# Kernel tuning notes

Measured on AMD Instinct MI355X. Metric: run time of the kernel, lower is better.

The kernel has to match this reference:

```python
import jax, jax.numpy as jnp
import numpy as np

KH, KW = 3, 3
KN = KH * KW  # kernel_n = 9


def _grid_offset(H, W):
    # Faithful to TF build(): stack(meshgrid(ij)).reshape(-1, 2) -- note this
    # interleaves i- and j- grids in an unusual layout; we replicate it exactly.
    init = jnp.stack(jnp.meshgrid(jnp.arange(KH), jnp.arange(KW), indexing='ij'))
    init = init.reshape(-1, 2).astype(jnp.float32)  # (KN, 2)
    ph, pw = (KH - 1) // 2, (KW - 1) // 2
    g = jnp.stack(
        jnp.meshgrid(jnp.arange(-ph, H - ph), jnp.arange(-pw, W - pw), indexing='ij'),
        axis=-1,
    ).astype(jnp.float32)  # (H, W, 2)
    return g[:, :, None, :] + init[None, None]  # (H, W, KN, 2)


def _bilinear_sample(x, coords):
    # x: (B, H, W, C); coords: (B, H, W, KN, 2) with (row, col) float coords.
    B = x.shape[0]
    y, xc = coords[..., 0], coords[..., 1]
    y0 = jnp.floor(y).astype(jnp.int32)
    y1 = jnp.ceil(y).astype(jnp.int32)   # ceil (not floor+1), faithful to TF code
    x0 = jnp.floor(xc).astype(jnp.int32)
    x1 = jnp.ceil(xc).astype(jnp.int32)
    bidx = jnp.arange(B)[:, None, None, None]

    def g(yy, xx):
        return x[bidx, yy, xx]  # (B, H, W, KN, C)

    v_lt = g(y0, x0)
    v_rb = g(y1, x1)
    v_lb = g(y0, x1)  # (lt_row, rb_col) per TF coords_lb
    v_rt = g(y1, x0)  # (rb_row, lt_col) per TF coords_rt
    fy = (y - y0.astype(y.dtype))[..., None]
    fx = (xc - x0.astype(xc.dtype))[..., None]
    v_t = v_lt + (v_rt - v_lt) * fy
    v_b = v_lb + (v_rb - v_lb) * fy
    return v_t + (v_b - v_t) * fx  # (B, H, W, KN, C)


def setup_inputs() -> dict:
    key = jax.random.key(0)
    k1, k2, k3 = jax.random.split(key, 3)
    B, H, W, C, F = 8, 64, 64, 128, 128
    x = jax.random.normal(k1, (B, H, W, C), dtype=jnp.float32)
    offset = jax.random.normal(k2, (B, H, W, 2 * KN), dtype=jnp.float32)
    Wk = jax.random.truncated_normal(k3, -2.0, 2.0, (KN, C, F), dtype=jnp.float32) * 0.02
    b = jnp.zeros((F,), dtype=jnp.float32)
    return {"x": x, "offset": offset, "W": Wk, "b": b}


def reference(x, offset, W, b):
    B, H, Wd, C = x.shape
    coords = _grid_offset(H, Wd)[None] + offset.reshape(B, H, Wd, KN, 2)
    coords = jnp.stack(
        [
            jnp.clip(coords[..., 0], 0.0, float(H - 1)),
            jnp.clip(coords[..., 1], 0.0, float(Wd - 1)),
        ],
        axis=-1,
    )
    deform = _bilinear_sample(x, coords)  # (B, H, W, KN, C)
    # conv3d with (1,1,KN,C,F) filter, VALID == contraction over (KN, C)
    out = jnp.einsum('bhwnc,ncf->bhwf', deform, W) + b
    return out
```

## Files before the change

kernel.cpp:

```cpp
#include <hip/hip_runtime.h>
#include <stdint.h>

#define KN 9
#define HH 64
#define WW 64
#define CC 128
#define FF 128
#define TM 64
#define NT 512
#define LDK 136

typedef __bf16 bf16x8 __attribute__((ext_vector_type(8)));
typedef float f32x4 __attribute__((ext_vector_type(4)));
typedef unsigned short us8 __attribute__((ext_vector_type(8)));
typedef unsigned short us4 __attribute__((ext_vector_type(4)));

__constant__ float c_init_i[KN] = {0.f,0.f,1.f,2.f,2.f,1.f,0.f,2.f,1.f};
__constant__ float c_init_j[KN] = {0.f,1.f,1.f,2.f,0.f,2.f,1.f,0.f,2.f};

static __device__ inline unsigned short f2bf(float f) {
    union { float f; unsigned u; } v; v.f = f;
    unsigned r = v.u + 0x7fffu + ((v.u >> 16) & 1u);
    return (unsigned short)(r >> 16);
}

__global__ void wt_kernel(const float* __restrict__ Wk, unsigned short* __restrict__ Wt) {
    __shared__ unsigned short t[32][33];
    const int tid = threadIdx.x;
    const int n  = blockIdx.x >> 4;
    const int tf = blockIdx.x & 3;
    const int tc = (blockIdx.x >> 2) & 3;
    const int g  = tid >> 5;
    const int l  = tid & 31;
#pragma unroll
    for (int r = 0; r < 4; ++r) {
        int cl = g * 4 + r;
        t[cl][l] = f2bf(Wk[(n << 14) + ((tc * 32 + cl) << 7) + (tf * 32 + l)]);
    }
    __syncthreads();
#pragma unroll
    for (int r = 0; r < 4; ++r) {
        int fl = g * 4 + r;
        Wt[(n << 14) + ((tf * 32 + fl) << 7) + (tc * 32 + l)] = t[l][fl];
    }
}

__launch_bounds__(NT, 4)
__global__ void deform_kernel(const float* __restrict__ xin,
                              const float* __restrict__ off,
                              const unsigned short* __restrict__ Wt,
                              const float* __restrict__ bias,
                              float* __restrict__ out) {
    __shared__ unsigned short As[TM][LDK];
    __shared__ unsigned short Bt[FF][LDK];
    __shared__ float cY[TM][KN];
    __shared__ float cX[TM][KN];

    const int tid = threadIdx.x;
    const int bb   = blockIdx.x & 7;
    const int hh   = blockIdx.x >> 3;
    const int pix0 = (bb << 12) + (hh << 6);

    for (int t = tid; t < TM * KN; t += NT) {
        int p = t & (TM - 1);
        int n = t >> 6;
        const float* op = off + (size_t)(pix0 + p) * (2 * KN) + 2 * n;
        float y = (float)(hh - 1) + c_init_i[n] + op[0];
        float x = (float)(p - 1) + c_init_j[n] + op[1];
        cY[p][n] = fminf(fmaxf(y, 0.f), 63.f);
        cX[p][n] = fminf(fmaxf(x, 0.f), 63.f);
    }
    __syncthreads();

    const int wave = tid >> 6;
    const int lane = tid & 63;
    const int quad = lane >> 4;
    const int col  = lane & 15;
    const int mtile = (wave & 1) * 32;
    const int ntile = (wave >> 1) * 32;

    f32x4 acc[2][2];
#pragma unroll
    for (int a = 0; a < 2; ++a)
#pragma unroll
        for (int b = 0; b < 2; ++b) acc[a][b] = (f32x4){0.f, 0.f, 0.f, 0.f};

    const float* bbase = xin + ((size_t)bb << 19);

    auto issue_gather = [&](int n, int k, float4* pf) {
        int i  = tid + k * NT;
        int p  = i >> 5;
        int cg = (i & 31) * 4;
        float y = cY[p][n], x = cX[p][n];
        int y0 = (int)floorf(y), x0 = (int)floorf(x);
        int y1 = (int)ceilf(y),  x1 = (int)ceilf(x);
        pf[0] = *(const float4*)(bbase + ((((y0 << 6) + x0) << 7) + cg));
        pf[1] = *(const float4*)(bbase + ((((y1 << 6) + x0) << 7) + cg));
        pf[2] = *(const float4*)(bbase + ((((y0 << 6) + x1) << 7) + cg));
        pf[3] = *(const float4*)(bbase + ((((y1 << 6) + x1) << 7) + cg));
    };
    auto consume = [&](int n, int k, const float4* pf) {
        int i  = tid + k * NT;
        int p  = i >> 5;
        int cg = (i & 31) * 4;
        float y = cY[p][n], x = cX[p][n];
        float fy = y - floorf(y), fx = x - floorf(x);
        float r0, r1, r2, r3;
        { float vt = pf[0].x + (pf[1].x - pf[0].x) * fy; float vb = pf[2].x + (pf[3].x - pf[2].x) * fy; r0 = vt + (vb - vt) * fx; }
        { float vt = pf[0].y + (pf[1].y - pf[0].y) * fy; float vb = pf[2].y + (pf[3].y - pf[2].y) * fy; r1 = vt + (vb - vt) * fx; }
        { float vt = pf[0].z + (pf[1].z - pf[0].z) * fy; float vb = pf[2].z + (pf[3].z - pf[2].z) * fy; r2 = vt + (vb - vt) * fx; }
        { float vt = pf[0].w + (pf[1].w - pf[0].w) * fy; float vb = pf[2].w + (pf[3].w - pf[2].w) * fy; r3 = vt + (vb - vt) * fx; }
        us4 pk;
        pk.x = f2bf(r0); pk.y = f2bf(r1); pk.z = f2bf(r2); pk.w = f2bf(r3);
        *(us4*)&As[p][cg] = pk;
    };

    float4 pf0[4], pf1[4];
    us8 bpf[4];
    issue_gather(0, 0, pf0);
    issue_gather(0, 1, pf1);
#pragma unroll
    for (int k = 0; k < 4; ++k) {
        int i2 = tid + k * NT;
        bpf[k] = *(const us8*)(Wt + (i2 >> 4) * CC + (i2 & 15) * 8);
    }

    for (int n = 0; n < KN; ++n) {
        float4 pf2[4], pf3[4];
        issue_gather(n, 2, pf2);
        issue_gather(n, 3, pf3);
#pragma unroll
        for (int k = 0; k < 4; ++k) {
            int i2 = tid + k * NT;
            *(us8*)&Bt[i2 >> 4][(i2 & 15) * 8] = bpf[k];
        }
        consume(n, 0, pf0);
        consume(n, 1, pf1);
        consume(n, 2, pf2);
        consume(n, 3, pf3);
        __syncthreads();

        if (n + 1 < KN) {
            issue_gather(n + 1, 0, pf0);
            issue_gather(n + 1, 1, pf1);
            const unsigned short* Wn = Wt + (n + 1) * (CC * FF);
#pragma unroll
            for (int k = 0; k < 4; ++k) {
                int i2 = tid + k * NT;
                bpf[k] = *(const us8*)(Wn + (i2 >> 4) * CC + (i2 & 15) * 8);
            }
        }

#pragma unroll
        for (int ks = 0; ks < 4; ++ks) {
            bf16x8 a0 = __builtin_bit_cast(bf16x8, *(const us8*)(&As[mtile + col][ks * 32 + quad * 8]));
            bf16x8 a1 = __builtin_bit_cast(bf16x8, *(const us8*)(&As[mtile + 16 + col][ks * 32 + quad * 8]));
            bf16x8 b0 = __builtin_bit_cast(bf16x8, *(const us8*)(&Bt[ntile + col][ks * 32 + quad * 8]));
            bf16x8 b1 = __builtin_bit_cast(bf16x8, *(const us8*)(&Bt[ntile + 16 + col][ks * 32 + quad * 8]));
            acc[0][0] = __builtin_amdgcn_mfma_f32_16x16x32_bf16(a0, b0, acc[0][0], 0, 0, 0);
            acc[0][1] = __builtin_amdgcn_mfma_f32_16x16x32_bf16(a0, b1, acc[0][1], 0, 0, 0);
            acc[1][0] = __builtin_amdgcn_mfma_f32_16x16x32_bf16(a1, b0, acc[1][0], 0, 0, 0);
            acc[1][1] = __builtin_amdgcn_mfma_f32_16x16x32_bf16(a1, b1, acc[1][1], 0, 0, 0);
        }
        __syncthreads();
    }

#pragma unroll
    for (int b = 0; b < 2; ++b) {
        int f = ntile + b * 16 + col;
        float bv = bias[f];
#pragma unroll
        for (int a = 0; a < 2; ++a) {
#pragma unroll
            for (int r = 0; r < 4; ++r) {
                int pr = pix0 + mtile + a * 16 + quad * 4 + r;
                out[(size_t)pr * FF + f] = acc[a][b][r] + bv;
            }
        }
    }
}

extern "C" void kernel_launch(void* const* d_in, const int* in_sizes, int n_in,
                              void* d_out, int out_size, void* d_ws, size_t ws_size,
                              hipStream_t stream) {
    const float* x    = (const float*)d_in[0];
    const float* off  = (const float*)d_in[1];
    const float* Wk   = (const float*)d_in[2];
    const float* bias = (const float*)d_in[3];
    float* out = (float*)d_out;
    unsigned short* Wt = (unsigned short*)d_ws;

    wt_kernel<<<KN * 16, 256, 0, stream>>>(Wk, Wt);
    deform_kernel<<<(8 * HH * WW) / TM, NT, 0, stream>>>(x, off, Wt, bias, out);
}
```

Baseline: 105.3 us.

## Load weights directly into registers and precompute gather offsets per tap

Repacks the bf16 weight workspace so each wave reads its MFMA B fragments straight from global memory into registers, which removes the shared-memory Bt tile and the store/read round trip through it. Corner offsets and fractional weights are now computed once in the prologue and kept in shared memory, so the gather loop no longer repeats floor/ceil per tap. Each thread now handles 8 channels of 2 pixels instead of 4 channels of 4 pixels, and uses native bf16 conversion. Less shared memory may allow more blocks per CU. In exchange, register pressure rises (16 float4 prefetch values plus 8 weight vectors), and the weight loads are now exposed in the main loop without prefetching across taps.

```diff
diff --git a/kernel.cpp b/kernel.cpp
--- a/kernel.cpp
+++ b/kernel.cpp
@@ -13,7 +13,6 @@
 typedef __bf16 bf16x8 __attribute__((ext_vector_type(8)));
 typedef float f32x4 __attribute__((ext_vector_type(4)));
 typedef unsigned short us8 __attribute__((ext_vector_type(8)));
-typedef unsigned short us4 __attribute__((ext_vector_type(4)));
 
 __constant__ float c_init_i[KN] = {0.f,0.f,1.f,2.f,2.f,1.f,0.f,2.f,1.f};
 __constant__ float c_init_j[KN] = {0.f,1.f,1.f,2.f,0.f,2.f,1.f,0.f,2.f};
@@ -41,7 +40,7 @@
 #pragma unroll
     for (int r = 0; r < 4; ++r) {
         int fl = g * 4 + r;
-        Wt[(n << 14) + ((tf * 32 + fl) << 7) + (tc * 32 + l)] = t[l][fl];
+        Wt[(n << 14) + (tc << 12) + ((tf * 32 + fl) << 5) + l] = t[l][fl];
     }
 }
 
@@ -52,9 +51,8 @@
                               const float* __restrict__ bias,
                               float* __restrict__ out) {
     __shared__ unsigned short As[TM][LDK];
-    __shared__ unsigned short Bt[FF][LDK];
-    __shared__ float cY[TM][KN];
-    __shared__ float cX[TM][KN];
+    __shared__ int   cB[TM][KN][4];
+    __shared__ float cF[TM][KN][2];
 
     const int tid = threadIdx.x;
     const int bb   = blockIdx.x & 7;
@@ -67,10 +65,18 @@
         const float* op = off + (size_t)(pix0 + p) * (2 * KN) + 2 * n;
         float y = (float)(hh - 1) + c_init_i[n] + op[0];
         float x = (float)(p - 1) + c_init_j[n] + op[1];
-        cY[p][n] = fminf(fmaxf(y, 0.f), 63.f);
-        cX[p][n] = fminf(fmaxf(x, 0.f), 63.f);
+        y = fminf(fmaxf(y, 0.f), 63.f);
+        x = fminf(fmaxf(x, 0.f), 63.f);
+        float y0f = floorf(y), x0f = floorf(x);
+        int y0 = (int)y0f, x0 = (int)x0f;
+        int y1 = (int)ceilf(y), x1 = (int)ceilf(x);
+        cB[p][n][0] = ((y0 << 6) + x0) << 7;
+        cB[p][n][1] = ((y1 << 6) + x0) << 7;
+        cB[p][n][2] = ((y0 << 6) + x1) << 7;
+        cB[p][n][3] = ((y1 << 6) + x1) << 7;
+        cF[p][n][0] = y - y0f;
+        cF[p][n][1] = x - x0f;
     }
-    __syncthreads();
 
     const int wave = tid >> 6;
     const int lane = tid & 63;
@@ -86,77 +92,66 @@
         for (int b = 0; b < 2; ++b) acc[a][b] = (f32x4){0.f, 0.f, 0.f, 0.f};
 
     const float* bbase = xin + ((size_t)bb << 19);
+    const unsigned short* wb0 = Wt + ((ntile + col) << 5) + (quad << 3);
 
-    auto issue_gather = [&](int n, int k, float4* pf) {
-        int i  = tid + k * NT;
-        int p  = i >> 5;
-        int cg = (i & 31) * 4;
-        float y = cY[p][n], x = cX[p][n];
-        int y0 = (int)floorf(y), x0 = (int)floorf(x);
-        int y1 = (int)ceilf(y),  x1 = (int)ceilf(x);
-        pf[0] = *(const float4*)(bbase + ((((y0 << 6) + x0) << 7) + cg));
-        pf[1] = *(const float4*)(bbase + ((((y1 << 6) + x0) << 7) + cg));
-        pf[2] = *(const float4*)(bbase + ((((y0 << 6) + x1) << 7) + cg));
-        pf[3] = *(const float4*)(bbase + ((((y1 << 6) + x1) << 7) + cg));
+    const int ip0 = tid >> 4;
+    const int ip1 = ip0 + 32;
+    const int icg = (tid & 15) * 8;
+
+    auto issue = [&](int n, int p, float4* pf) {
+        int4 cb = *(const int4*)&cB[p][n][0];
+        const float* c0 = bbase + cb.x + icg;
+        const float* c1 = bbase + cb.y + icg;
+        const float* c2 = bbase + cb.z + icg;
+        const float* c3 = bbase + cb.w + icg;
+        pf[0] = *(const float4*)c0; pf[1] = *(const float4*)(c0 + 4);
+        pf[2] = *(const float4*)c1; pf[3] = *(const float4*)(c1 + 4);
+        pf[4] = *(const float4*)c2; pf[5] = *(const float4*)(c2 + 4);
+        pf[6] = *(const float4*)c3; pf[7] = *(const float4*)(c3 + 4);
     };
-    auto consume = [&](int n, int k, const float4* pf) {
-        int i  = tid + k * NT;
-        int p  = i >> 5;
-        int cg = (i & 31) * 4;
-        float y = cY[p][n], x = cX[p][n];
-        float fy = y - floorf(y), fx = x - floorf(x);
-        float r0, r1, r2, r3;
-        { float vt = pf[0].x + (pf[1].x - pf[0].x) * fy; float vb = pf[2].x + (pf[3].x - pf[2].x) * fy; r0 = vt + (vb - vt) * fx; }
-        { float vt = pf[0].y + (pf[1].y - pf[0].y) * fy; float vb = pf[2].y + (pf[3].y - pf[2].y) * fy; r1 = vt + (vb - vt) * fx; }
-        { float vt = pf[0].z + (pf[1].z - pf[0].z) * fy; float vb = pf[2].z + (pf[3].z - pf[2].z) * fy; r2 = vt + (vb - vt) * fx; }
-        { float vt = pf[0].w + (pf[1].w - pf[0].w) * fy; float vb = pf[2].w + (pf[3].w - pf[2].w) * fy; r3 = vt + (vb - vt) * fx; }
-        us4 pk;
-        pk.x = f2bf(r0); pk.y = f2bf(r1); pk.z = f2bf(r2); pk.w = f2bf(r3);
-        *(us4*)&As[p][cg] = pk;
+    auto consume = [&](int n, int p, const float4* pf) {
+        float fy = cF[p][n][0], fx = cF[p][n][1];
+        us8 pk;
+#pragma unroll
+        for (int j = 0; j < 8; ++j) {
+            float v0 = pf[0 + (j >> 2)][j & 3];
+            float v1 = pf[2 + (j >> 2)][j & 3];
+            float v2 = pf[4 + (j >> 2)][j & 3];
+            float v3 = pf[6 + (j >> 2)][j & 3];
+            float vt = v0 + (v1 - v0) * fy;
+            float vb = v2 + (v3 - v2) * fy;
+            float r  = vt + (vb - vt) * fx;
+            pk[j] = __builtin_bit_cast(unsigned short, (__bf16)r);
+        }
+        *(us8*)&As[p][icg] = pk;
     };
 
-    float4 pf0[4], pf1[4];
-    us8 bpf[4];
-    issue_gather(0, 0, pf0);
-    issue_gather(0, 1, pf1);
-#pragma unroll
-    for (int k = 0; k < 4; ++k) {
-        int i2 = tid + k * NT;
-        bpf[k] = *(const us8*)(Wt + (i2 >> 4) * CC + (i2 & 15) * 8);
-    }
+    __syncthreads();
+
+    float4 pf0[8], pf1[8];
+    us8 bfr[8];
+    issue(0, ip0, pf0);
 
     for (int n = 0; n < KN; ++n) {
-        float4 pf2[4], pf3[4];
-        issue_gather(n, 2, pf2);
-        issue_gather(n, 3, pf3);
+        const unsigned short* wn = wb0 + (n << 14);
 #pragma unroll
-        for (int k = 0; k < 4; ++k) {
-            int i2 = tid + k * NT;
-            *(us8*)&Bt[i2 >> 4][(i2 & 15) * 8] = bpf[k];
+        for (int ks = 0; ks < 4; ++ks) {
+            bfr[ks * 2]     = *(const us8*)(wn + (ks << 12));
+            bfr[ks * 2 + 1] = *(const us8*)(wn + (ks << 12) + (16 << 5));
         }
-        consume(n, 0, pf0);
-        consume(n, 1, pf1);
-        consume(n, 2, pf2);
-        consume(n, 3, pf3);
+        issue(n, ip1, pf1);
+        consume(n, ip0, pf0);
+        consume(n, ip1, pf1);
         __syncthreads();
 
-        if (n + 1 < KN) {
-            issue_gather(n + 1, 0, pf0);
-            issue_gather(n + 1, 1, pf1);
-            const unsigned short* Wn = Wt + (n + 1) * (CC * FF);
-#pragma unroll
-            for (int k = 0; k < 4; ++k) {
-                int i2 = tid + k * NT;
-                bpf[k] = *(const us8*)(Wn + (i2 >> 4) * CC + (i2 & 15) * 8);
-            }
-        }
+        if (n + 1 < KN) issue(n + 1, ip0, pf0);
 
 #pragma unroll
         for (int ks = 0; ks < 4; ++ks) {
             bf16x8 a0 = __builtin_bit_cast(bf16x8, *(const us8*)(&As[mtile + col][ks * 32 + quad * 8]));
             bf16x8 a1 = __builtin_bit_cast(bf16x8, *(const us8*)(&As[mtile + 16 + col][ks * 32 + quad * 8]));
-            bf16x8 b0 = __builtin_bit_cast(bf16x8, *(const us8*)(&Bt[ntile + col][ks * 32 + quad * 8]));
-            bf16x8 b1 = __builtin_bit_cast(bf16x8, *(const us8*)(&Bt[ntile + 16 + col][ks * 32 + quad * 8]));
+            bf16x8 b0 = __builtin_bit_cast(bf16x8, bfr[ks * 2]);
+            bf16x8 b1 = __builtin_bit_cast(bf16x8, bfr[ks * 2 + 1]);
             acc[0][0] = __builtin_amdgcn_mfma_f32_16x16x32_bf16(a0, b0, acc[0][0], 0, 0, 0);
             acc[0][1] = __builtin_amdgcn_mfma_f32_16x16x32_bf16(a0, b1, acc[0][1], 0, 0, 0);
             acc[1][0] = __builtin_amdgcn_mfma_f32_16x16x32_bf16(a1, b0, acc[1][0], 0, 0, 0);
```

Result: slower. 110.2 us (+4.6%).
